# Performance work log

Measured on AMD Instinct MI355X. Metric: run time of the kernel, lower is better.

Reference implementation:

```python
import jax, jax.numpy as jnp
import numpy as np

TAU = 30.0
EPS = 1e-5

def layernorm(x, gamma, beta):
    mu = jnp.mean(x, axis=-1, keepdims=True)
    var = jnp.var(x, axis=-1, keepdims=True)
    return (x - mu) * jax.lax.rsqrt(var + EPS) * gamma + beta

def setup_inputs() -> dict:
    key = jax.random.key(0)
    ks = jax.random.split(key, 10)
    B, L, D, H, E = 2, 2048, 768, 12, 64
    x = jax.random.normal(ks[0], (B, L, D), dtype=jnp.float32)
    attention_mask = jnp.ones((B, L), dtype=jnp.int32)
    # stacked per-head projection weights, each head: (d_head, d_model)
    WQ = jax.random.normal(ks[1], (H, E, D), dtype=jnp.float32)
    WK = jax.random.normal(ks[2], (H, E, D), dtype=jnp.float32)
    WV = jax.random.normal(ks[3], (H, E, D), dtype=jnp.float32)
    gamma1 = jnp.ones((D,), jnp.float32); beta1 = jnp.zeros((D,), jnp.float32)
    gamma2 = jnp.ones((D,), jnp.float32); beta2 = jnp.zeros((D,), jnp.float32)
    W_O = jax.random.normal(ks[4], (D, D), dtype=jnp.float32)
    W_up = jax.random.normal(ks[5], (D, H * D), dtype=jnp.float32) * 0.02
    b_up = jnp.zeros((H * D,), jnp.float32)
    W_down = jax.random.normal(ks[6], (H * D, D), dtype=jnp.float32) * 0.02
    b_down = jnp.zeros((D,), jnp.float32)
    return {"x": x, "attention_mask": attention_mask, "WQ": WQ, "WK": WK, "WV": WV,
            "gamma1": gamma1, "beta1": beta1, "gamma2": gamma2, "beta2": beta2,
            "W_O": W_O, "W_up": W_up, "b_up": b_up, "W_down": W_down, "b_down": b_down}

def reference(x, attention_mask, WQ, WK, WV, gamma1, beta1, gamma2, beta2,
              W_O, W_up, b_up, W_down, b_down):
    B, L, D = x.shape
    E = WQ.shape[1]
    u = layernorm(x, gamma1, beta1)
    # per-head projections: (B, H, L, E)
    Q = jnp.einsum('bld,hed->bhle', u, WQ)
    K = jnp.einsum('bld,hed->bhle', u, WK)
    V = jnp.einsum('bld,hed->bhle', u, WV)
    S = jnp.einsum('bhle,bhme->bhlm', Q, K) / jnp.sqrt(jnp.float32(E))
    S = TAU * jnp.tanh(S)  # mode == 'tanh-clipped'
    causal = jnp.triu(jnp.ones((L, L), dtype=bool), k=1)  # True above diagonal
    S = jnp.where(causal, -jnp.inf, S)
    pad = (attention_mask == 0)[:, None, None, :]  # (B,1,1,L) key mask
    S = jnp.where(pad, -jnp.inf, S)
    A = jax.nn.softmax(S, axis=-1)
    O = jnp.einsum('bhlm,bhme->bhle', A, V)  # (B,H,L,E)
    heads_cat = O.transpose(0, 2, 1, 3).reshape(B, L, -1)  # (B,L,H*E)
    attn = heads_cat @ W_O.T
    z1 = x + attn
    v1 = layernorm(z1, gamma2, beta2)
    v3 = jax.nn.gelu(v1 @ W_up + b_up, approximate=False)
    z2 = z1 + v3 @ W_down + b_down
    return z2
```

## Files before the change

### kernel.cpp

```cpp
#include <hip/hip_runtime.h>
#include <stdint.h>

typedef __attribute__((ext_vector_type(8))) short bf16x8;
typedef __attribute__((ext_vector_type(4))) float f32x4;
typedef __attribute__((ext_vector_type(4))) unsigned short us4;
typedef unsigned short ushort;
typedef unsigned int uint;

#define MFMA16(a,b,c) __builtin_amdgcn_mfma_f32_16x16x32_bf16((a),(b),(c),0,0,0)

__device__ __forceinline__ ushort f2bf(float f){
  uint u = __builtin_bit_cast(uint, f);
  return (ushort)((u + 0x7fffu + ((u>>16)&1u)) >> 16);
}
__device__ __forceinline__ float bf2f(ushort h){
  return __builtin_bit_cast(float, ((uint)h)<<16);
}
__device__ __forceinline__ void gll16(const void* g, void* l){
  __builtin_amdgcn_global_load_lds((const __attribute__((address_space(1))) void*)g,
                                   (__attribute__((address_space(3))) void*)l, 16, 0, 0);
}

template<bool SPLIT, int BK>
__device__ __forceinline__ void gemm_core(
    const char* __restrict__ Ah, const char* __restrict__ Al,
    const char* __restrict__ Bh, const char* __restrict__ Bl,
    int K, int lda, int ldb, int m0, int n0,
    f32x4 acc[4][4], char* sAh, char* sAl, char* sBh, char* sBl)
{
  constexpr int ROWB = BK*2;
  constexpr int CHUNKS = 128*ROWB/1024;
  constexpr int XM = ((ROWB/16)-1) & 7;
  const int tid = threadIdx.x;
  const int wave = tid>>6, lane = tid&63;
  const int l15 = lane&15, l4 = lane>>4;
  const int wr = (wave>>1)*64, wc = (wave&1)*64;
  const int nsteps = K / BK;
  for (int kt = 0; kt < nsteps; ++kt) {
    const int kb0 = kt*ROWB;
    for (int c = wave; c < CHUNKS; c += 4) {
      const int p = (c<<10) + (lane<<4);
      const int row = p / ROWB;
      const int gk = (p % ROWB) ^ ((row & XM)<<4);
      gll16(Ah + (size_t)(m0+row)*lda + kb0 + gk, sAh + (c<<10));
      gll16(Bh + (size_t)(n0+row)*ldb + kb0 + gk, sBh + (c<<10));
      if constexpr (SPLIT) {
        gll16(Al + (size_t)(m0+row)*lda + kb0 + gk, sAl + (c<<10));
        gll16(Bl + (size_t)(n0+row)*ldb + kb0 + gk, sBl + (c<<10));
      }
    }
    __syncthreads();
    #pragma unroll
    for (int ks = 0; ks < BK/32; ++ks) {
      bf16x8 ah[4], bh_[4], al[4], bl[4];
      #pragma unroll
      for (int i = 0; i < 4; ++i) {
        const int ar = wr + i*16 + l15;
        const int ao = ar*ROWB + ((ks*64 + l4*16) ^ ((ar & XM)<<4));
        ah[i] = *(const bf16x8*)(sAh + ao);
        const int br = wc + i*16 + l15;
        const int bo = br*ROWB + ((ks*64 + l4*16) ^ ((br & XM)<<4));
        bh_[i] = *(const bf16x8*)(sBh + bo);
        if constexpr (SPLIT) {
          al[i] = *(const bf16x8*)(sAl + ao);
          bl[i] = *(const bf16x8*)(sBl + bo);
        }
      }
      #pragma unroll
      for (int mi = 0; mi < 4; ++mi) {
        #pragma unroll
        for (int ni = 0; ni < 4; ++ni) {
          acc[mi][ni] = MFMA16(ah[mi], bh_[ni], acc[mi][ni]);
          if constexpr (SPLIT) {
            acc[mi][ni] = MFMA16(ah[mi], bl[ni], acc[mi][ni]);
            acc[mi][ni] = MFMA16(al[mi], bh_[ni], acc[mi][ni]);
          }
        }
      }
    }
    __syncthreads();
  }
}

__global__ __launch_bounds__(256) void k_prep(
    const float* __restrict__ wq, const float* __restrict__ wk,
    const float* __restrict__ wv, const float* __restrict__ wo,
    ushort* qh, ushort* ql_, ushort* kh, ushort* kl_, ushort* vb, ushort* ob)
{
  int i = blockIdx.x*256 + threadIdx.x;
  if (i >= 589824) return;
  float a = wq[i]; ushort h = f2bf(a); qh[i]=h; ql_[i]=f2bf(a - bf2f(h));
  float b = wk[i]; h = f2bf(b); kh[i]=h; kl_[i]=f2bf(b - bf2f(h));
  vb[i] = f2bf(wv[i]); ob[i] = f2bf(wo[i]);
}

__global__ __launch_bounds__(256) void k_transpose(
    const float* __restrict__ in, ushort* __restrict__ out, int R, int C)
{
  __shared__ float t[32][33];
  const int bx = blockIdx.x*32, by = blockIdx.y*32;
  const int tx = threadIdx.x & 31, ty = threadIdx.x >> 5;
  #pragma unroll
  for (int i = 0; i < 4; ++i)
    t[ty + i*8][tx] = in[(size_t)(by + ty + i*8)*C + bx + tx];
  __syncthreads();
  #pragma unroll
  for (int i = 0; i < 4; ++i)
    out[(size_t)(bx + ty + i*8)*R + by + tx] = f2bf(t[tx][ty + i*8]);
}

__global__ __launch_bounds__(256) void k_ln(
    const float* __restrict__ in, const float* __restrict__ g, const float* __restrict__ be,
    ushort* __restrict__ oh, ushort* __restrict__ ol)
{
  const int row = blockIdx.x, t = threadIdx.x;
  const float* r = in + (size_t)row*768;
  float v0 = r[t], v1 = r[t+256], v2 = r[t+512];
  float s = v0+v1+v2;
  float q = v0*v0 + v1*v1 + v2*v2;
  #pragma unroll
  for (int m = 32; m; m >>= 1) { s += __shfl_xor(s, m); q += __shfl_xor(q, m); }
  __shared__ float ss[4], sq[4];
  const int wave = t>>6, lane = t&63;
  if (!lane) { ss[wave] = s; sq[wave] = q; }
  __syncthreads();
  s = ss[0]+ss[1]+ss[2]+ss[3];
  q = sq[0]+sq[1]+sq[2]+sq[3];
  const float mu = s*(1.f/768.f);
  const float var = q*(1.f/768.f) - mu*mu;
  const float inv = rsqrtf(var + 1e-5f);
  const float vv[3] = {v0, v1, v2};
  #pragma unroll
  for (int i = 0; i < 3; ++i) {
    const int idx = t + i*256;
    const float u = (vv[i]-mu)*inv*g[idx] + be[idx];
    const ushort hi = f2bf(u);
    oh[(size_t)row*768 + idx] = hi;
    if (ol) ol[(size_t)row*768 + idx] = f2bf(u - bf2f(hi));
  }
}

__global__ __launch_bounds__(256) void k_qkv(
    const ushort* __restrict__ uh, const ushort* __restrict__ ul,
    const ushort* __restrict__ wqh, const ushort* __restrict__ wql,
    const ushort* __restrict__ wkh, const ushort* __restrict__ wkl,
    const ushort* __restrict__ wvb,
    ushort* __restrict__ Qh, ushort* __restrict__ Ql,
    ushort* __restrict__ Kh, ushort* __restrict__ Kl,
    ushort* __restrict__ Vt)
{
  __shared__ char sA[8192], sA2[8192], sB[8192], sB2[8192];
  const int z = blockIdx.z;
  const int m0 = blockIdx.x*128, n0 = blockIdx.y*128;
  f32x4 acc[4][4] = {};
  if (z == 0)
    gemm_core<true,32>((const char*)uh, (const char*)ul, (const char*)wqh, (const char*)wql,
                       768, 1536, 1536, m0, n0, acc, sA, sA2, sB, sB2);
  else if (z == 1)
    gemm_core<true,32>((const char*)uh, (const char*)ul, (const char*)wkh, (const char*)wkl,
                       768, 1536, 1536, m0, n0, acc, sA, sA2, sB, sB2);
  else
    gemm_core<false,32>((const char*)uh, nullptr, (const char*)wvb, nullptr,
                        768, 1536, 1536, m0, n0, acc, sA, sA2, sB, sB2);

  const int tid = threadIdx.x, wave = tid>>6, lane = tid&63;
  const int l15 = lane&15, l4 = lane>>4;
  const int wr = (wave>>1)*64, wc = (wave&1)*64;
  if (z < 2) {
    ushort* __restrict__ Oh = z ? Kh : Qh;
    ushort* __restrict__ Ol = z ? Kl : Ql;
    #pragma unroll
    for (int mi = 0; mi < 4; ++mi) {
      #pragma unroll
      for (int ni = 0; ni < 4; ++ni) {
        const int he = n0 + wc + ni*16 + l15;
        const int h = he>>6, e = he&63;
        #pragma unroll
        for (int r = 0; r < 4; ++r) {
          const int n = m0 + wr + mi*16 + l4*4 + r;
          const int b = n>>11, l = n&2047;
          const size_t dst = ((size_t)((b*12+h)*2048 + l))*64 + e;
          const float c = acc[mi][ni][r];
          const ushort hi = f2bf(c);
          Oh[dst] = hi;
          Ol[dst] = f2bf(c - bf2f(hi));
        }
      }
    }
  } else {
    #pragma unroll
    for (int mi = 0; mi < 4; ++mi) {
      #pragma unroll
      for (int ni = 0; ni < 4; ++ni) {
        const int he = n0 + wc + ni*16 + l15;
        const int h = he>>6, e = he&63;
        const int n = m0 + wr + mi*16 + l4*4;
        const int b = n>>11, l = n&2047;
        us4 v;
        #pragma unroll
        for (int r = 0; r < 4; ++r) v[r] = f2bf(acc[mi][ni][r]);
        *(us4*)(Vt + ((size_t)((b*12+h)*64 + e))*2048 + l) = v;
      }
    }
  }
}

__global__ __launch_bounds__(256) void k_attn(
    const ushort* __restrict__ Qh, const ushort* __restrict__ Ql,
    const ushort* __restrict__ Kh, const ushort* __restrict__ Kl,
    const ushort* __restrict__ Vt, const int* __restrict__ am,
    ushort* __restrict__ Oc)
{
  __shared__ char sKh[8192], sKl[8192], sV[8192];
  __shared__ char sP[4][2048];
  const int qt = gridDim.x - 1 - blockIdx.x;
  const int bh = blockIdx.y;
  const int b = bh / 12, h = bh - b*12;
  const int tid = threadIdx.x, wave = tid>>6, lane = tid&63;
  const int l15 = lane&15, l4 = lane>>4;

  const size_t qoff = ((size_t)bh*2048 + qt*64 + wave*16 + l15)*64 + l4*8;
  const bf16x8 q_h0 = *(const bf16x8*)(Qh + qoff);
  const bf16x8 q_h1 = *(const bf16x8*)(Qh + qoff + 32);
  const bf16x8 q_l0 = *(const bf16x8*)(Ql + qoff);
  const bf16x8 q_l1 = *(const bf16x8*)(Ql + qoff + 32);

  f32x4 oacc[4] = {};
  float dsum[4] = {0.f, 0.f, 0.f, 0.f};
  const char* Kh_t = (const char*)(Kh + (size_t)bh*2048*64);
  const char* Kl_t = (const char*)(Kl + (size_t)bh*2048*64);
  const char* Vt_b = (const char*)(Vt + (size_t)bh*64*2048);

  for (int kt = 0; kt <= qt; ++kt) {
    for (int c = wave; c < 24; c += 4) {
      const int p = ((c&7)<<10) + (lane<<4);
      const int row = p >> 7;
      const int gkb = (p & 127) ^ ((row&7)<<4);
      const char* gsrc; char* lbase;
      if (c < 8)       { gsrc = Kh_t + (size_t)(kt*64+row)*128 + gkb; lbase = sKh + ((c&7)<<10); }
      else if (c < 16) { gsrc = Kl_t + (size_t)(kt*64+row)*128 + gkb; lbase = sKl + ((c&7)<<10); }
      else             { gsrc = Vt_b + (size_t)row*4096 + kt*128 + gkb; lbase = sV + ((c&7)<<10); }
      gll16(gsrc, lbase);
    }
    __syncthreads();

    f32x4 s[4] = {};
    #pragma unroll
    for (int ks = 0; ks < 2; ++ks) {
      bf16x8 kbh[4], kbl[4];
      #pragma unroll
      for (int nt = 0; nt < 4; ++nt) {
        const int key = nt*16 + l15;
        const int byte = key*128 + ((ks*64 + l4*16) ^ ((key&7)<<4));
        kbh[nt] = *(const bf16x8*)(sKh + byte);
        kbl[nt] = *(const bf16x8*)(sKl + byte);
      }
      const bf16x8 qh_ = ks ? q_h1 : q_h0;
      const bf16x8 ql_ = ks ? q_l1 : q_l0;
      #pragma unroll
      for (int nt = 0; nt < 4; ++nt) {
        s[nt] = MFMA16(qh_, kbh[nt], s[nt]);
        s[nt] = MFMA16(qh_, kbl[nt], s[nt]);
        s[nt] = MFMA16(ql_, kbh[nt], s[nt]);
      }
    }

    const bool diag = (kt == qt);
    #pragma unroll
    for (int nt = 0; nt < 4; ++nt) {
      const int key_g = kt*64 + nt*16 + l15;
      const float mv = (float)am[b*2048 + key_g];
      #pragma unroll
      for (int r = 0; r < 4; ++r) {
        const float sv = s[nt][r]*0.125f;
        const float th = 1.f - 2.f/(1.f + __expf(2.f*sv));
        float p = __expf(30.f*th - 30.f) * mv;
        if (diag && key_g > qt*64 + wave*16 + l4*4 + r) p = 0.f;
        dsum[r] += p;
        const int qi = l4*4 + r;
        const int byte = qi*128 + ((nt*32 + l15*2) ^ ((qi&7)<<4));
        *(ushort*)(sP[wave] + byte) = f2bf(p);
      }
    }

    #pragma unroll
    for (int ks = 0; ks < 2; ++ks) {
      const int abyte = l15*128 + ((ks*64 + l4*16) ^ ((l15&7)<<4));
      const bf16x8 pa = *(const bf16x8*)(sP[wave] + abyte);
      #pragma unroll
      for (int et = 0; et < 4; ++et) {
        const int e_l = et*16 + l15;
        const int vbyte = e_l*128 + ((ks*64 + l4*16) ^ ((e_l&7)<<4));
        const bf16x8 vb = *(const bf16x8*)(sV + vbyte);
        oacc[et] = MFMA16(pa, vb, oacc[et]);
      }
    }
    __syncthreads();
  }

  #pragma unroll
  for (int r = 0; r < 4; ++r) {
    float d = dsum[r];
    d += __shfl_xor(d, 1); d += __shfl_xor(d, 2);
    d += __shfl_xor(d, 4); d += __shfl_xor(d, 8);
    dsum[r] = 1.f/d;
  }
  #pragma unroll
  for (int et = 0; et < 4; ++et) {
    #pragma unroll
    for (int r = 0; r < 4; ++r) {
      const int q_g = qt*64 + wave*16 + l4*4 + r;
      const size_t n = (size_t)b*2048 + q_g;
      const int he = h*64 + et*16 + l15;
      Oc[n*768 + he] = f2bf(oacc[et][r]*dsum[r]);
    }
  }
}

__global__ __launch_bounds__(256) void k_wo(
    const ushort* __restrict__ oc, const ushort* __restrict__ wob,
    const float* __restrict__ x, float* __restrict__ z1)
{
  __shared__ char sA[16384], sB[16384];
  const int m0 = blockIdx.x*128, n0 = blockIdx.y*128;
  f32x4 acc[4][4] = {};
  gemm_core<false,64>((const char*)oc, nullptr, (const char*)wob, nullptr,
                      768, 1536, 1536, m0, n0, acc, sA, nullptr, sB, nullptr);
  const int tid = threadIdx.x, wave = tid>>6, lane = tid&63;
  const int l15 = lane&15, l4 = lane>>4;
  const int wr = (wave>>1)*64, wc = (wave&1)*64;
  #pragma unroll
  for (int mi = 0; mi < 4; ++mi) {
    #pragma unroll
    for (int ni = 0; ni < 4; ++ni) {
      const int d = n0 + wc + ni*16 + l15;
      #pragma unroll
      for (int r = 0; r < 4; ++r) {
        const int n = m0 + wr + mi*16 + l4*4 + r;
        z1[(size_t)n*768 + d] = x[(size_t)n*768 + d] + acc[mi][ni][r];
      }
    }
  }
}

__global__ __launch_bounds__(256) void k_up(
    const ushort* __restrict__ v1, const ushort* __restrict__ wupT,
    const float* __restrict__ bup, ushort* __restrict__ v3)
{
  __shared__ char sA[16384], sB[16384];
  const int m0 = blockIdx.x*128, n0 = blockIdx.y*128;
  f32x4 acc[4][4] = {};
  gemm_core<false,64>((const char*)v1, nullptr, (const char*)wupT, nullptr,
                      768, 1536, 1536, m0, n0, acc, sA, nullptr, sB, nullptr);
  const int tid = threadIdx.x, wave = tid>>6, lane = tid&63;
  const int l15 = lane&15, l4 = lane>>4;
  const int wr = (wave>>1)*64, wc = (wave&1)*64;
  #pragma unroll
  for (int mi = 0; mi < 4; ++mi) {
    #pragma unroll
    for (int ni = 0; ni < 4; ++ni) {
      const int j = n0 + wc + ni*16 + l15;
      const float bj = bup[j];
      #pragma unroll
      for (int r = 0; r < 4; ++r) {
        const int n = m0 + wr + mi*16 + l4*4 + r;
        const float c = acc[mi][ni][r] + bj;
        const float ge = 0.5f*c*(1.f + erff(c*0.70710678118654752f));
        v3[(size_t)n*9216 + j] = f2bf(ge);
      }
    }
  }
}

__global__ __launch_bounds__(256) void k_down(
    const ushort* __restrict__ v3, const ushort* __restrict__ wdnT,
    const float* __restrict__ z1, const float* __restrict__ bdn,
    float* __restrict__ out)
{
  __shared__ char sA[16384], sB[16384];
  const int m0 = blockIdx.x*128, n0 = blockIdx.y*128;
  f32x4 acc[4][4] = {};
  gemm_core<false,64>((const char*)v3, nullptr, (const char*)wdnT, nullptr,
                      9216, 18432, 18432, m0, n0, acc, sA, nullptr, sB, nullptr);
  const int tid = threadIdx.x, wave = tid>>6, lane = tid&63;
  const int l15 = lane&15, l4 = lane>>4;
  const int wr = (wave>>1)*64, wc = (wave&1)*64;
  #pragma unroll
  for (int mi = 0; mi < 4; ++mi) {
    #pragma unroll
    for (int ni = 0; ni < 4; ++ni) {
      const int d = n0 + wc + ni*16 + l15;
      const float bd = bdn[d];
      #pragma unroll
      for (int r = 0; r < 4; ++r) {
        const int n = m0 + wr + mi*16 + l4*4 + r;
        out[(size_t)n*768 + d] = z1[(size_t)n*768 + d] + acc[mi][ni][r] + bd;
      }
    }
  }
}

extern "C" void kernel_launch(void* const* d_in, const int* in_sizes, int n_in,
                              void* d_out, int out_size, void* d_ws, size_t ws_size,
                              hipStream_t stream) {
  const float* x   = (const float*)d_in[0];
  const int*   am  = (const int*)d_in[1];
  const float* WQ  = (const float*)d_in[2];
  const float* WK  = (const float*)d_in[3];
  const float* WV  = (const float*)d_in[4];
  const float* g1  = (const float*)d_in[5];
  const float* b1  = (const float*)d_in[6];
  const float* g2  = (const float*)d_in[7];
  const float* b2  = (const float*)d_in[8];
  const float* WO  = (const float*)d_in[9];
  const float* Wup = (const float*)d_in[10];
  const float* bup = (const float*)d_in[11];
  const float* Wdn = (const float*)d_in[12];
  const float* bdn = (const float*)d_in[13];
  float* out = (float*)d_out;

  char* w = (char*)d_ws;
  ushort* wqh  = (ushort*)(w + 0);
  ushort* wql  = (ushort*)(w + 1179648);
  ushort* wkh  = (ushort*)(w + 2359296);
  ushort* wkl  = (ushort*)(w + 3538944);
  ushort* wvb  = (ushort*)(w + 4718592);
  ushort* wob  = (ushort*)(w + 5898240);
  ushort* wupT = (ushort*)(w + 7077888);
  ushort* wdnT = (ushort*)(w + 21233664);
  float*  z1   = (float*) (w + 35389440);
  ushort* v1h  = (ushort*)(w + 47972352);
  char*  pool  = w + 54263808;
  ushort* uh   = (ushort*)(pool + 0);
  ushort* ul   = (ushort*)(pool + 6291456);
  ushort* Qh_  = (ushort*)(pool + 12582912);
  ushort* Ql_  = (ushort*)(pool + 18874368);
  ushort* Kh_  = (ushort*)(pool + 25165824);
  ushort* Kl_  = (ushort*)(pool + 31457280);
  ushort* Vt_  = (ushort*)(pool + 37748736);
  ushort* oc   = (ushort*)(pool + 44040192);
  ushort* v3   = (ushort*)(pool + 0);
  const size_t NEED = 54263808u + 75497472u;
  if (ws_size < NEED) return;

  k_prep<<<2304, 256, 0, stream>>>(WQ, WK, WV, WO, wqh, wql, wkh, wkl, wvb, wob);
  k_transpose<<<dim3(288, 24), 256, 0, stream>>>(Wup, wupT, 768, 9216);
  k_transpose<<<dim3(24, 288), 256, 0, stream>>>(Wdn, wdnT, 9216, 768);
  k_ln<<<4096, 256, 0, stream>>>(x, g1, b1, uh, ul);
  k_qkv<<<dim3(32, 6, 3), 256, 0, stream>>>(uh, ul, wqh, wql, wkh, wkl, wvb,
                                            Qh_, Ql_, Kh_, Kl_, Vt_);
  k_attn<<<dim3(32, 24), 256, 0, stream>>>(Qh_, Ql_, Kh_, Kl_, Vt_, am, oc);
  k_wo<<<dim3(32, 6), 256, 0, stream>>>(oc, wob, x, z1);
  k_ln<<<4096, 256, 0, stream>>>(z1, g2, b2, v1h, nullptr);
  k_up<<<dim3(32, 72), 256, 0, stream>>>(v1h, wupT, bup, v3);
  k_down<<<dim3(32, 6), 256, 0, stream>>>(v3, wdnT, z1, bdn, out);
}
```

Measured before the change: 556.1 us.

## Split-K the W_O and down-projection GEMMs with atomic accumulation

The W_O GEMM is split into 2 K-slices and the down-projection GEMM into 4 K-slices. Each slice atomically adds its partial tile into an output buffer that is pre-initialised, either by a device memcpy of x or by a new bias-plus-residual init kernel. The point is to fill more CUs, since the original grids had only 192 blocks. The attention softmax exponent is also simplified algebraically, from 30*tanh-30 to -60/(1+e^{2s}). The cost is extra atomic traffic, an extra memcpy and kernel launch, and non-deterministic summation order.

```diff
diff --git a/kernel.cpp b/kernel.cpp
--- a/kernel.cpp
+++ b/kernel.cpp
@@ -273,8 +273,7 @@
       #pragma unroll
       for (int r = 0; r < 4; ++r) {
         const float sv = s[nt][r]*0.125f;
-        const float th = 1.f - 2.f/(1.f + __expf(2.f*sv));
-        float p = __expf(30.f*th - 30.f) * mv;
+        float p = __expf(-60.f/(1.f + __expf(2.f*sv))) * mv;
         if (diag && key_g > qt*64 + wave*16 + l4*4 + r) p = 0.f;
         dsum[r] += p;
         const int qi = l4*4 + r;
@@ -319,13 +318,14 @@
 
 __global__ __launch_bounds__(256) void k_wo(
     const ushort* __restrict__ oc, const ushort* __restrict__ wob,
-    const float* __restrict__ x, float* __restrict__ z1)
+    float* __restrict__ z1)
 {
   __shared__ char sA[16384], sB[16384];
   const int m0 = blockIdx.x*128, n0 = blockIdx.y*128;
+  const int kz = blockIdx.z;
   f32x4 acc[4][4] = {};
-  gemm_core<false,64>((const char*)oc, nullptr, (const char*)wob, nullptr,
-                      768, 1536, 1536, m0, n0, acc, sA, nullptr, sB, nullptr);
+  gemm_core<false,64>((const char*)oc + kz*768, nullptr, (const char*)wob + kz*768, nullptr,
+                      384, 1536, 1536, m0, n0, acc, sA, nullptr, sB, nullptr);
   const int tid = threadIdx.x, wave = tid>>6, lane = tid&63;
   const int l15 = lane&15, l4 = lane>>4;
   const int wr = (wave>>1)*64, wc = (wave&1)*64;
@@ -337,7 +337,7 @@
       #pragma unroll
       for (int r = 0; r < 4; ++r) {
         const int n = m0 + wr + mi*16 + l4*4 + r;
-        z1[(size_t)n*768 + d] = x[(size_t)n*768 + d] + acc[mi][ni][r];
+        unsafeAtomicAdd(&z1[(size_t)n*768 + d], acc[mi][ni][r]);
       }
     }
   }
@@ -372,16 +372,28 @@
   }
 }
 
+__global__ __launch_bounds__(256) void k_oinit(
+    const float* __restrict__ z1, const float* __restrict__ bdn, float* __restrict__ out)
+{
+  const int i = blockIdx.x*256 + threadIdx.x;
+  const f32x4 z = *(const f32x4*)(z1 + (size_t)i*4);
+  const int d = (i*4) % 768;
+  f32x4 o;
+  #pragma unroll
+  for (int j = 0; j < 4; ++j) o[j] = z[j] + bdn[d+j];
+  *(f32x4*)(out + (size_t)i*4) = o;
+}
+
 __global__ __launch_bounds__(256) void k_down(
     const ushort* __restrict__ v3, const ushort* __restrict__ wdnT,
-    const float* __restrict__ z1, const float* __restrict__ bdn,
     float* __restrict__ out)
 {
   __shared__ char sA[16384], sB[16384];
   const int m0 = blockIdx.x*128, n0 = blockIdx.y*128;
+  const int kz = blockIdx.z;
   f32x4 acc[4][4] = {};
-  gemm_core<false,64>((const char*)v3, nullptr, (const char*)wdnT, nullptr,
-                      9216, 18432, 18432, m0, n0, acc, sA, nullptr, sB, nullptr);
+  gemm_core<false,64>((const char*)v3 + kz*4608, nullptr, (const char*)wdnT + kz*4608, nullptr,
+                      2304, 18432, 18432, m0, n0, acc, sA, nullptr, sB, nullptr);
   const int tid = threadIdx.x, wave = tid>>6, lane = tid&63;
   const int l15 = lane&15, l4 = lane>>4;
   const int wr = (wave>>1)*64, wc = (wave&1)*64;
@@ -390,11 +402,10 @@
     #pragma unroll
     for (int ni = 0; ni < 4; ++ni) {
       const int d = n0 + wc + ni*16 + l15;
-      const float bd = bdn[d];
       #pragma unroll
       for (int r = 0; r < 4; ++r) {
         const int n = m0 + wr + mi*16 + l4*4 + r;
-        out[(size_t)n*768 + d] = z1[(size_t)n*768 + d] + acc[mi][ni][r] + bd;
+        unsafeAtomicAdd(&out[(size_t)n*768 + d], acc[mi][ni][r]);
       }
     }
   }
@@ -450,8 +461,10 @@
   k_qkv<<<dim3(32, 6, 3), 256, 0, stream>>>(uh, ul, wqh, wql, wkh, wkl, wvb,
                                             Qh_, Ql_, Kh_, Kl_, Vt_);
   k_attn<<<dim3(32, 24), 256, 0, stream>>>(Qh_, Ql_, Kh_, Kl_, Vt_, am, oc);
-  k_wo<<<dim3(32, 6), 256, 0, stream>>>(oc, wob, x, z1);
+  hipMemcpyAsync(z1, x, 12582912, hipMemcpyDeviceToDevice, stream);
+  k_wo<<<dim3(32, 6, 2), 256, 0, stream>>>(oc, wob, z1);
   k_ln<<<4096, 256, 0, stream>>>(z1, g2, b2, v1h, nullptr);
   k_up<<<dim3(32, 72), 256, 0, stream>>>(v1h, wupT, bup, v3);
-  k_down<<<dim3(32, 6), 256, 0, stream>>>(v3, wdnT, z1, bdn, out);
-}
+  k_oinit<<<3072, 256, 0, stream>>>(z1, bdn, out);
+  k_down<<<dim3(32, 6, 4), 256, 0, stream>>>(v3, wdnT, out);
+}
```

After: 530.9 us. 1.05x faster.
